# Kernel tuning notes

Measured on AMD Instinct MI355X. Metric: run time of the kernel, lower is better.

## Reference

```python
import jax, jax.numpy as jnp
import numpy as np
import math

B, S, D = 8, 4096, 64

def setup_inputs() -> dict:
    key = jax.random.key(0)
    k1, k2, k3 = jax.random.split(key, 3)
    value = jax.random.normal(k1, (B, S, D), dtype=jnp.float32)
    key_t = jax.random.normal(k2, (B, S, D), dtype=jnp.float32)
    query = jax.random.normal(k3, (B, S, D), dtype=jnp.float32)
    return {"value": value, "key": key_t, "query": query}

def reference(value, key, query):
    # scores[b, q, k] = sum_d query[b,q,d] * key[b,k,d]
    scores = jnp.einsum('bqd,bkd->bqk', query, key) / math.sqrt(query.shape[-1])
    # NOTE: softmax over dim=1 (the QUERY axis), matching the original torch code
    attn = jax.nn.softmax(scores, axis=1)
    # outputs[b, q, d] = sum_k attn[b,q,k] * value[b,k,d]
    return jnp.einsum('bqk,bkd->bqd', attn, value)
```

## Files before the change

kernel.cpp:

```cpp
#include <hip/hip_runtime.h>

#define Bn 8
#define Sn 4096
#define Dn 64

constexpr int NKT = Sn / 64;
constexpr int NQT = Sn / 128;

typedef _Float16 half_t;
typedef __attribute__((ext_vector_type(2))) _Float16 half2v;
typedef __attribute__((ext_vector_type(4))) _Float16 half4;
typedef __attribute__((ext_vector_type(8))) _Float16 half8;
typedef __attribute__((ext_vector_type(4))) float f32x4;

constexpr float SCALE = 0.125f;
constexpr float SCALE2 = 0.125f * 1.4426950408889634f;

#define MFMA32(a, b, c) __builtin_amdgcn_mfma_f32_16x16x32_f16((a), (b), (c), 0, 0, 0)
#define MFMA16(a, b, c) __builtin_amdgcn_mfma_f32_16x16x16f16((a), (b), (c), 0, 0, 0)

__device__ __forceinline__ float fexp2(float x) {
#if defined(__has_builtin) && __has_builtin(__builtin_amdgcn_exp2f)
  return __builtin_amdgcn_exp2f(x);
#else
  return exp2f(x);
#endif
}

__device__ __forceinline__ int swz_k(int row, int col) {
  return row * 64 + (col ^ ((row & 7) << 3));
}
__device__ __forceinline__ int swz_v(int row, int col) {
  return row * 64 + (col ^ (((row & 7) << 3) ^ (((row >> 3) & 7) << 2)));
}

__device__ __forceinline__ void cvt8(const float* s, half8& h, half8& l) {
  #pragma unroll
  for (int j = 0; j < 8; ++j) {
    half_t hh = (half_t)s[j];
    h[j] = hh;
    l[j] = (half_t)(s[j] - (float)hh);
  }
}

__device__ __forceinline__ void cp16(half_t* lds, const half_t* g) {
  __builtin_amdgcn_global_load_lds(
      (const __attribute__((address_space(1))) unsigned int*)g,
      (__attribute__((address_space(3))) unsigned int*)lds, 16, 0, 0);
}


__global__ __launch_bounds__(256, 2)
void prep_q(const float* __restrict__ Qg, half_t* __restrict__ QhW,
            half_t* __restrict__ QlW) {
  const int t = threadIdx.x;
  const int b = blockIdx.x & 7, qt = blockIdx.x >> 3;
  const float* Qb = Qg + ((size_t)(b * Sn + qt * 128)) * Dn;
  half_t* qh = QhW + ((size_t)(b * NQT + qt)) * 8192;
  half_t* ql = QlW + ((size_t)(b * NQT + qt)) * 8192;
  #pragma unroll
  for (int i = 0; i < 8; ++i) {
    int f = t + 256 * i, q = f >> 4, d4 = (f & 15) << 2;
    float4 v = *(const float4*)(Qb + (size_t)q * Dn + d4);
    float s4[4] = {v.x * SCALE2, v.y * SCALE2, v.z * SCALE2, v.w * SCALE2};
    half4 h, l;
    #pragma unroll
    for (int j = 0; j < 4; ++j) {
      half_t hh = (half_t)s4[j];
      h[j] = hh;
      l[j] = (half_t)(s4[j] - (float)hh);
    }
    *(half4*)&qh[swz_k(q, d4)] = h;
    *(half4*)&ql[swz_k(q, d4)] = l;
  }
}

__global__ __launch_bounds__(256, 2)
void attn_linv(const float* __restrict__ Kg, const float* __restrict__ Vg,
               const half_t* __restrict__ QhW, const half_t* __restrict__ QlW,
               float* __restrict__ lg2inv, half_t* __restrict__ KVW) {
  __shared__ alignas(16) half_t Qh_s[2][8192];
  __shared__ alignas(16) half_t Ql_s[2][8192];
  __shared__ alignas(16) float red[4][4][16];

  const int t = threadIdx.x;
  const int lane = t & 63, w = t >> 6, g = lane >> 4, c16 = lane & 15;
  const int b = blockIdx.x & 7, kx = blockIdx.x >> 3;
  const int k0 = kx * 64;

  half_t* blob = KVW + ((size_t)(b * NKT + kx)) * 12288;

  half8 kfh[4][2], kfl[4][2];
  #pragma unroll
  for (int ks = 0; ks < 4; ++ks)
    #pragma unroll
    for (int c = 0; c < 2; ++c) {
      const float* src = Kg + ((size_t)(b * Sn + k0 + 16 * ks + c16)) * Dn + 32 * c + 8 * g;
      float a8[8];
      *(float4*)&a8[0] = *(const float4*)src;
      *(float4*)&a8[4] = *(const float4*)(src + 4);
      cvt8(a8, kfh[ks][c], kfl[ks][c]);
    }
  {
    #pragma unroll
    for (int ks = 0; ks < 4; ++ks)
      if (ks == w) {
        #pragma unroll
        for (int c = 0; c < 2; ++c) {
          *(half8*)&blob[swz_k(16 * ks + c16, 32 * c + 8 * g)] = kfh[ks][c];
          *(half8*)&blob[4096 + swz_k(16 * ks + c16, 32 * c + 8 * g)] = kfl[ks][c];
        }
      }
  }
  {
    const float* Vb = Vg + ((size_t)(b * Sn + k0)) * Dn;
    #pragma unroll
    for (int i = 0; i < 2; ++i) {
      int u = t + 256 * i;
      int k2 = u >> 4, dg = u & 15;
      float4 v0 = *(const float4*)(Vb + (size_t)(2 * k2) * Dn + 4 * dg);
      float4 v1 = *(const float4*)(Vb + (size_t)(2 * k2 + 1) * Dn + 4 * dg);
      const float* v0p = (const float*)&v0;
      const float* v1p = (const float*)&v1;
      #pragma unroll
      for (int j = 0; j < 4; ++j) {
        half2v pair = {(half_t)v0p[j], (half_t)v1p[j]};
        *(half2v*)&blob[8192 + swz_v(4 * dg + j, 2 * k2)] = pair;
      }
    }
  }

  const half_t* qhw = QhW + (size_t)b * NQT * 8192;
  const half_t* qlw = QlW + (size_t)b * NQT * 8192;

  auto load_q = [&](int bb, int qt) {
    const size_t toff = (size_t)qt * 8192;
    #pragma unroll
    for (int c = 0; c < 4; ++c) {
      const int ch = (c * 4 + w) * 512;
      cp16(&Qh_s[bb][ch], qhw + toff + ch + lane * 8);
      cp16(&Ql_s[bb][ch], qlw + toff + ch + lane * 8);
    }
  };

  float lsum[4] = {0.f, 0.f, 0.f, 0.f};

  load_q(0, 0);
  __syncthreads();
  for (int qt = 0; qt < NQT; ++qt) {
    if (qt + 1 < NQT) load_q((qt + 1) & 1, qt + 1);
    const int cur = qt & 1;
    #pragma unroll
    for (int qs = 0; qs < 2; ++qs) {
      const int qloc = 32 * w + 16 * qs + c16;
      half8 qh[2], ql[2];
      #pragma unroll
      for (int c = 0; c < 2; ++c) {
        qh[c] = *(const half8*)&Qh_s[cur][swz_k(qloc, 32 * c + 8 * g)];
        ql[c] = *(const half8*)&Ql_s[cur][swz_k(qloc, 32 * c + 8 * g)];
      }
      #pragma unroll
      for (int ks = 0; ks < 4; ++ks) {
        f32x4 acc = {0.f, 0.f, 0.f, 0.f};
        acc = MFMA32(qh[0], kfh[ks][0], acc);
        acc = MFMA32(qh[1], kfh[ks][1], acc);
        acc = MFMA32(ql[0], kfh[ks][0], acc);
        acc = MFMA32(ql[1], kfh[ks][1], acc);
        acc = MFMA32(qh[0], kfl[ks][0], acc);
        acc = MFMA32(qh[1], kfl[ks][1], acc);
        lsum[ks] += fexp2(acc[0]) + fexp2(acc[1]) + fexp2(acc[2]) + fexp2(acc[3]);
      }
    }
    __syncthreads();
  }

  #pragma unroll
  for (int ks = 0; ks < 4; ++ks) {
    lsum[ks] += __shfl_xor(lsum[ks], 16);
    lsum[ks] += __shfl_xor(lsum[ks], 32);
  }
  __syncthreads();
  if (lane < 16) {
    #pragma unroll
    for (int ks = 0; ks < 4; ++ks) red[w][ks][lane] = lsum[ks];
  }
  __syncthreads();
  if (t < 64) {
    int ks = t >> 4, c = t & 15;
    float tot = red[0][ks][c] + red[1][ks][c] + red[2][ks][c] + red[3][ks][c];
    lg2inv[(size_t)b * Sn + k0 + 16 * ks + c] = -log2f(tot);
  }
}

__global__ __launch_bounds__(512, 4)
void attn_pv(const half_t* __restrict__ KVW, const float* __restrict__ Qg,
             const float* __restrict__ lg2inv, float* __restrict__ Og) {
  __shared__ alignas(16) half_t KV_s[2][12288];

  const int t = threadIdx.x;
  const int lane = t & 63, w = t >> 6;
  const int g = (lane >> 4) & 3, c16 = lane & 15;
  const int wk = w & 3, wq = w >> 2;
  const int b = blockIdx.x & 7;
  const int q0 = (blockIdx.x >> 3) * 64;

  half8 qh[2][2], ql[2][2];
  #pragma unroll
  for (int qs = 0; qs < 2; ++qs) {
    const int qrow = q0 + 32 * wq + 16 * qs + c16;
    #pragma unroll
    for (int c = 0; c < 2; ++c) {
      const float* src = Qg + ((size_t)(b * Sn + qrow)) * Dn + 32 * c + 8 * g;
      float a8[8];
      *(float4*)&a8[0] = *(const float4*)src;
      *(float4*)&a8[4] = *(const float4*)(src + 4);
      #pragma unroll
      for (int j = 0; j < 8; ++j) a8[j] *= SCALE2;
      cvt8(a8, qh[qs][c], ql[qs][c]);
    }
  }

  f32x4 accO[2][4];
  #pragma unroll
  for (int qs = 0; qs < 2; ++qs)
    #pragma unroll
    for (int ds = 0; ds < 4; ++ds) accO[qs][ds] = {0.f, 0.f, 0.f, 0.f};

  auto load_kv = [&](int bb, int kt) {
    const half_t* src = KVW + ((size_t)(b * NKT + kt)) * 12288;
    half_t* dst = KV_s[bb];
    cp16(dst + w * 512, src + w * 512 + lane * 8);
    cp16(dst + (8 + w) * 512, src + (8 + w) * 512 + lane * 8);
    cp16(dst + (16 + w) * 512, src + (16 + w) * 512 + lane * 8);
  };

  const int krow = 16 * wk + c16;
  const int okh0 = swz_k(krow, 8 * g);
  const int okh1 = swz_k(krow, 32 + 8 * g);
  const float* lgp = lg2inv + (size_t)b * Sn + 16 * wk + 4 * g;

  load_kv(0, 0);
  __syncthreads();
  for (int kt = 0; kt < NKT; ++kt) {
    if (kt + 1 < NKT) load_kv((kt + 1) & 1, kt + 1);
    const int cur = kt & 1;
    const half_t* KH = &KV_s[cur][0];
    const half_t* KL = &KV_s[cur][4096];
    const half_t* VT = &KV_s[cur][8192];

    half8 kh0 = *(const half8*)&KH[okh0];
    half8 kh1 = *(const half8*)&KH[okh1];
    half8 kl0 = *(const half8*)&KL[okh0];
    half8 kl1 = *(const half8*)&KL[okh1];
    f32x4 lg4 = *(const f32x4*)(lgp + (size_t)kt * 64);

    f32x4 sv[2];
    __builtin_amdgcn_s_setprio(1);
    #pragma unroll
    for (int qs = 0; qs < 2; ++qs) {
      f32x4 acc = {0.f, 0.f, 0.f, 0.f};
      acc = MFMA32(kh0, qh[qs][0], acc);
      acc = MFMA32(kh1, qh[qs][1], acc);
      acc = MFMA32(kh0, ql[qs][0], acc);
      acc = MFMA32(kh1, ql[qs][1], acc);
      acc = MFMA32(kl0, qh[qs][0], acc);
      acc = MFMA32(kl1, qh[qs][1], acc);
      sv[qs] = acc;
    }
    __builtin_amdgcn_s_setprio(0);

    half4 ph[2];
    #pragma unroll
    for (int qs = 0; qs < 2; ++qs) {
      float p0 = fexp2(sv[qs][0] + lg4[0]);
      float p1 = fexp2(sv[qs][1] + lg4[1]);
      float p2 = fexp2(sv[qs][2] + lg4[2]);
      float p3 = fexp2(sv[qs][3] + lg4[3]);
      ph[qs] = {(half_t)p0, (half_t)p1, (half_t)p2, (half_t)p3};
    }

    __builtin_amdgcn_s_setprio(1);
    #pragma unroll
    for (int ds = 0; ds < 4; ++ds) {
      half4 vt = *(const half4*)&VT[swz_v(16 * ds + c16, 16 * wk + 4 * g)];
      accO[0][ds] = MFMA16(vt, ph[0], accO[0][ds]);
      accO[1][ds] = MFMA16(vt, ph[1], accO[1][ds]);
    }
    __builtin_amdgcn_s_setprio(0);

    __syncthreads();
  }

  float* red = (float*)&KV_s[0][0];
  #pragma unroll
  for (int qs = 0; qs < 2; ++qs) {
    if (wk != 0) {
      #pragma unroll
      for (int ds = 0; ds < 4; ++ds)
        *(f32x4*)&red[(((wq * 3 + (wk - 1)) * 4) + ds) * 256 + lane * 4] = accO[qs][ds];
    }
    __syncthreads();
    if (wk == 0) {
      const int qrow = q0 + 32 * wq + 16 * qs + c16;
      float* Ob = Og + ((size_t)(b * Sn + qrow)) * Dn;
      #pragma unroll
      for (int ds = 0; ds < 4; ++ds) {
        f32x4 o = accO[qs][ds];
        #pragma unroll
        for (int j = 0; j < 3; ++j)
          o += *(const f32x4*)&red[(((wq * 3 + j) * 4) + ds) * 256 + lane * 4];
        *(f32x4*)(Ob + 16 * ds + 4 * g) = o;
      }
    }
    __syncthreads();
  }
}

__global__ __launch_bounds__(256, 2)
void fb_attn_linv(const float* __restrict__ Kg, const float* __restrict__ Qg,
                  float* __restrict__ linv) {
  __shared__ alignas(16) half_t Qh_s[128 * 64];
  __shared__ alignas(16) half_t Ql_s[128 * 64];
  __shared__ alignas(16) float red[4][4][16];

  const int t = threadIdx.x;
  const int lane = t & 63, w = t >> 6, g = lane >> 4, c16 = lane & 15;
  const int b = blockIdx.y;
  const int k0 = blockIdx.x * 64;

  half8 kfh[4][2], kfl[4][2];
  #pragma unroll
  for (int ks = 0; ks < 4; ++ks)
    #pragma unroll
    for (int c = 0; c < 2; ++c) {
      const float* src = Kg + ((size_t)(b * Sn + k0 + 16 * ks + c16)) * Dn + 32 * c + 8 * g;
      float a8[8];
      *(float4*)&a8[0] = *(const float4*)src;
      *(float4*)&a8[4] = *(const float4*)(src + 4);
      cvt8(a8, kfh[ks][c], kfl[ks][c]);
    }

  float lsum[4] = {0.f, 0.f, 0.f, 0.f};

  for (int q0 = 0; q0 < Sn; q0 += 128) {
    __syncthreads();
    const float* Qb = Qg + ((size_t)(b * Sn + q0)) * Dn;
    #pragma unroll
    for (int i = 0; i < 8; ++i) {
      int f = t + 256 * i, q = f >> 4, d4 = (f & 15) << 2;
      float4 v = *(const float4*)(Qb + (size_t)q * Dn + d4);
      float s4[4] = {v.x * SCALE, v.y * SCALE, v.z * SCALE, v.w * SCALE};
      half4 h, l;
      #pragma unroll
      for (int j = 0; j < 4; ++j) {
        half_t hh = (half_t)s4[j];
        h[j] = hh;
        l[j] = (half_t)(s4[j] - (float)hh);
      }
      *(half4*)&Qh_s[swz_k(q, d4)] = h;
      *(half4*)&Ql_s[swz_k(q, d4)] = l;
    }
    __syncthreads();

    #pragma unroll
    for (int qs = 0; qs < 2; ++qs) {
      const int qloc = 32 * w + 16 * qs + c16;
      half8 qh[2], ql[2];
      #pragma unroll
      for (int c = 0; c < 2; ++c) {
        qh[c] = *(const half8*)&Qh_s[swz_k(qloc, 32 * c + 8 * g)];
        ql[c] = *(const half8*)&Ql_s[swz_k(qloc, 32 * c + 8 * g)];
      }
      #pragma unroll
      for (int ks = 0; ks < 4; ++ks) {
        f32x4 acc = {0.f, 0.f, 0.f, 0.f};
        acc = MFMA32(qh[0], kfh[ks][0], acc);
        acc = MFMA32(qh[1], kfh[ks][1], acc);
        acc = MFMA32(ql[0], kfh[ks][0], acc);
        acc = MFMA32(ql[1], kfh[ks][1], acc);
        acc = MFMA32(qh[0], kfl[ks][0], acc);
        acc = MFMA32(qh[1], kfl[ks][1], acc);
        lsum[ks] += __expf(acc[0]) + __expf(acc[1]) + __expf(acc[2]) + __expf(acc[3]);
      }
    }
  }

  #pragma unroll
  for (int ks = 0; ks < 4; ++ks) {
    lsum[ks] += __shfl_xor(lsum[ks], 16);
    lsum[ks] += __shfl_xor(lsum[ks], 32);
  }
  __syncthreads();
  if (lane < 16) {
    #pragma unroll
    for (int ks = 0; ks < 4; ++ks) red[w][ks][lane] = lsum[ks];
  }
  __syncthreads();
  if (t < 64) {
    int ks = t >> 4, c = t & 15;
    float tot = red[0][ks][c] + red[1][ks][c] + red[2][ks][c] + red[3][ks][c];
    linv[(size_t)b * Sn + k0 + 16 * ks + c] = 1.0f / tot;
  }
}

__global__ __launch_bounds__(512, 2)
void fb_attn_pv(const float* __restrict__ Vg, const float* __restrict__ Kg,
                const float* __restrict__ Qg, const float* __restrict__ linv,
                float* __restrict__ Og) {
  __shared__ alignas(16) half_t Kh_s[64 * 64];
  __shared__ alignas(16) half_t Kl_s[64 * 64];
  __shared__ alignas(16) half_t Vt_s[64 * 64];
  __shared__ alignas(16) float li_s[64];
  __shared__ alignas(16) float red[4][2][4][256];

  const int t = threadIdx.x;
  const int lane = t & 63, w = t >> 6;
  const int g = (lane >> 4) & 3, c16 = lane & 15;
  const int wq = w & 3, wk = w >> 2;
  const int b = blockIdx.y;
  const int q0 = blockIdx.x * 128;

  half8 qh[2][2], ql[2][2];
  #pragma unroll
  for (int qs = 0; qs < 2; ++qs) {
    const int qrow = q0 + 32 * wq + 16 * qs + c16;
    #pragma unroll
    for (int c = 0; c < 2; ++c) {
      const float* src = Qg + ((size_t)(b * Sn + qrow)) * Dn + 32 * c + 8 * g;
      float a8[8];
      *(float4*)&a8[0] = *(const float4*)src;
      *(float4*)&a8[4] = *(const float4*)(src + 4);
      #pragma unroll
      for (int j = 0; j < 8; ++j) a8[j] *= SCALE;
      cvt8(a8, qh[qs][c], ql[qs][c]);
    }
  }

  f32x4 accO[2][4];
  #pragma unroll
  for (int qs = 0; qs < 2; ++qs)
    #pragma unroll
    for (int ds = 0; ds < 4; ++ds) accO[qs][ds] = {0.f, 0.f, 0.f, 0.f};

  const int krow0 = t >> 4, kd40 = (t & 15) << 2;
  const int krow1 = 32 + (t >> 4), kd41 = kd40;
  const int vk2 = t >> 4, vdg = t & 15;

  float4 kreg0, kreg1, vreg0, vreg1;
  float li_reg = 0.f;
  {
    const float* Kb = Kg + ((size_t)(b * Sn)) * Dn;
    const float* Vb = Vg + ((size_t)(b * Sn)) * Dn;
    kreg0 = *(const float4*)(Kb + (size_t)krow0 * Dn + kd40);
    kreg1 = *(const float4*)(Kb + (size_t)krow1 * Dn + kd41);
    vreg0 = *(const float4*)(Vb + (size_t)(2 * vk2) * Dn + 4 * vdg);
    vreg1 = *(const float4*)(Vb + (size_t)(2 * vk2 + 1) * Dn + 4 * vdg);
    if (t < 64) li_reg = linv[(size_t)b * Sn + t];
  }

  for (int kt = 0; kt < Sn / 64; ++kt) {
    __syncthreads();
    {
      const float* k0p = (const float*)&kreg0;
      const float* k1p = (const float*)&kreg1;
      half4 h, l;
      #pragma unroll
      for (int j = 0; j < 4; ++j) {
        half_t hh = (half_t)k0p[j];
        h[j] = hh; l[j] = (half_t)(k0p[j] - (float)hh);
      }
      *(half4*)&Kh_s[swz_k(krow0, kd40)] = h;
      *(half4*)&Kl_s[swz_k(krow0, kd40)] = l;
      #pragma unroll
      for (int j = 0; j < 4; ++j) {
        half_t hh = (half_t)k1p[j];
        h[j] = hh; l[j] = (half_t)(k1p[j] - (float)hh);
      }
      *(half4*)&Kh_s[swz_k(krow1, kd41)] = h;
      *(half4*)&Kl_s[swz_k(krow1, kd41)] = l;

      const float* v0p = (const float*)&vreg0;
      const float* v1p = (const float*)&vreg1;
      #pragma unroll
      for (int j = 0; j < 4; ++j) {
        half2v pair = {(half_t)v0p[j], (half_t)v1p[j]};
        *(half2v*)&Vt_s[swz_v(4 * vdg + j, 2 * vk2)] = pair;
      }
      if (t < 64) li_s[t] = li_reg;
    }
    __syncthreads();

    if (kt + 1 < Sn / 64) {
      const float* Kb = Kg + ((size_t)(b * Sn + (kt + 1) * 64)) * Dn;
      const float* Vb = Vg + ((size_t)(b * Sn + (kt + 1) * 64)) * Dn;
      kreg0 = *(const float4*)(Kb + (size_t)krow0 * Dn + kd40);
      kreg1 = *(const float4*)(Kb + (size_t)krow1 * Dn + kd41);
      vreg0 = *(const float4*)(Vb + (size_t)(2 * vk2) * Dn + 4 * vdg);
      vreg1 = *(const float4*)(Vb + (size_t)(2 * vk2 + 1) * Dn + 4 * vdg);
      if (t < 64) li_reg = linv[(size_t)b * Sn + (kt + 1) * 64 + t];
    }

    #pragma unroll
    for (int kss = 0; kss < 2; ++kss) {
      const int ks = 2 * wk + kss;
      const int krow = 16 * ks + c16;
      half8 kh0 = *(const half8*)&Kh_s[swz_k(krow, 8 * g)];
      half8 kh1 = *(const half8*)&Kh_s[swz_k(krow, 32 + 8 * g)];
      half8 kl0 = *(const half8*)&Kl_s[swz_k(krow, 8 * g)];
      half8 kl1 = *(const half8*)&Kl_s[swz_k(krow, 32 + 8 * g)];
      f32x4 li4 = *(const f32x4*)&li_s[16 * ks + 4 * g];

      half4 ph[2];
      #pragma unroll
      for (int qs = 0; qs < 2; ++qs) {
        f32x4 acc = {0.f, 0.f, 0.f, 0.f};
        acc = MFMA32(kh0, qh[qs][0], acc);
        acc = MFMA32(kh1, qh[qs][1], acc);
        acc = MFMA32(kh0, ql[qs][0], acc);
        acc = MFMA32(kh1, ql[qs][1], acc);
        acc = MFMA32(kl0, qh[qs][0], acc);
        acc = MFMA32(kl1, qh[qs][1], acc);
        float p0 = __expf(acc[0]) * li4[0];
        float p1 = __expf(acc[1]) * li4[1];
        float p2 = __expf(acc[2]) * li4[2];
        float p3 = __expf(acc[3]) * li4[3];
        ph[qs] = {(half_t)p0, (half_t)p1, (half_t)p2, (half_t)p3};
      }
      #pragma unroll
      for (int ds = 0; ds < 4; ++ds) {
        half4 vt = *(const half4*)&Vt_s[swz_v(16 * ds + c16, 16 * ks + 4 * g)];
        accO[0][ds] = MFMA16(vt, ph[0], accO[0][ds]);
        accO[1][ds] = MFMA16(vt, ph[1], accO[1][ds]);
      }
    }
  }

  if (wk == 1) {
    #pragma unroll
    for (int qs = 0; qs < 2; ++qs)
      #pragma unroll
      for (int ds = 0; ds < 4; ++ds)
        *(f32x4*)&red[wq][qs][ds][lane * 4] = accO[qs][ds];
  }
  __syncthreads();
  if (wk == 0) {
    #pragma unroll
    for (int qs = 0; qs < 2; ++qs) {
      const int qrow = q0 + 32 * wq + 16 * qs + c16;
      float* Ob = Og + ((size_t)(b * Sn + qrow)) * Dn;
      #pragma unroll
      for (int ds = 0; ds < 4; ++ds) {
        f32x4 o = accO[qs][ds] + *(const f32x4*)&red[wq][qs][ds][lane * 4];
        *(f32x4*)(Ob + 16 * ds + 4 * g) = o;
      }
    }
  }
}

extern "C" void kernel_launch(void* const* d_in, const int* in_sizes, int n_in,
                              void* d_out, int out_size, void* d_ws, size_t ws_size,
                              hipStream_t stream) {
  const float* V = reinterpret_cast<const float*>(d_in[0]);
  const float* K = reinterpret_cast<const float*>(d_in[1]);
  const float* Q = reinterpret_cast<const float*>(d_in[2]);
  float* O = reinterpret_cast<float*>(d_out);

  char* ws = reinterpret_cast<char*>(d_ws);
  const size_t MB = 1024 * 1024;
  const size_t WS_NEEDED = 21 * MB;

  float* li = reinterpret_cast<float*>(ws);
  if (ws_size >= WS_NEEDED) {
    half_t* QhW = reinterpret_cast<half_t*>(ws + 1 * MB);
    half_t* QlW = reinterpret_cast<half_t*>(ws + 5 * MB);
    half_t* KVW = reinterpret_cast<half_t*>(ws + 9 * MB);
    prep_q<<<dim3(NQT * Bn), dim3(256), 0, stream>>>(Q, QhW, QlW);
    attn_linv<<<dim3(NKT * Bn), dim3(256), 0, stream>>>(K, V, QhW, QlW, li, KVW);
    attn_pv<<<dim3((Sn / 64) * Bn), dim3(512), 0, stream>>>(KVW, Q, li, O);
  } else {
    fb_attn_linv<<<dim3(Sn / 64, Bn), dim3(256), 0, stream>>>(K, Q, li);
    fb_attn_pv<<<dim3(Sn / 128, Bn), dim3(512), 0, stream>>>(V, K, Q, li, O);
  }
}
```

Measured before the change: 133.4 us.

## Give each wave a private KV slice and drop per-tile block barriers

Reorganizes the packed K/V tile layout so each 16-key group forms a contiguous per-wave slice. In the PV kernel, each wave now streams its own slice into a double-buffered LDS region and waits only on its own async copies via s_waitcnt vmcnt, removing the __syncthreads at every key tile. The cost is doubled LDS per block, duplicate global loads for the two waves that share a key group, one wasted wrap-around prefetch, and a launch bound lowered from 4 to 2 blocks, which reduces occupancy.

```diff
diff --git a/kernel.cpp b/kernel.cpp
--- a/kernel.cpp
+++ b/kernel.cpp
@@ -107,8 +107,9 @@
       if (ks == w) {
         #pragma unroll
         for (int c = 0; c < 2; ++c) {
-          *(half8*)&blob[swz_k(16 * ks + c16, 32 * c + 8 * g)] = kfh[ks][c];
-          *(half8*)&blob[4096 + swz_k(16 * ks + c16, 32 * c + 8 * g)] = kfl[ks][c];
+          const int off = c16 * 64 + ((32 * c + 8 * g) ^ ((c16 & 7) << 3));
+          *(half8*)&blob[ks * 3072 + off] = kfh[ks][c];
+          *(half8*)&blob[ks * 3072 + 1024 + off] = kfl[ks][c];
         }
       }
   }
@@ -122,10 +123,12 @@
       float4 v1 = *(const float4*)(Vb + (size_t)(2 * k2 + 1) * Dn + 4 * dg);
       const float* v0p = (const float*)&v0;
       const float* v1p = (const float*)&v1;
+      const int wk = k2 >> 3;
+      const int kloc = (2 * k2) & 15;
       #pragma unroll
       for (int j = 0; j < 4; ++j) {
         half2v pair = {(half_t)v0p[j], (half_t)v1p[j]};
-        *(half2v*)&blob[8192 + swz_v(4 * dg + j, 2 * k2)] = pair;
+        *(half2v*)&blob[wk * 3072 + 2048 + (4 * dg + j) * 16 + kloc] = pair;
       }
     }
   }
@@ -192,10 +195,10 @@
   }
 }
 
-__global__ __launch_bounds__(512, 4)
+__global__ __launch_bounds__(512, 2)
 void attn_pv(const half_t* __restrict__ KVW, const float* __restrict__ Qg,
              const float* __restrict__ lg2inv, float* __restrict__ Og) {
-  __shared__ alignas(16) half_t KV_s[2][12288];
+  __shared__ alignas(16) half_t KV_s[2][24576];
 
   const int t = threadIdx.x;
   const int lane = t & 63, w = t >> 6;
@@ -203,6 +206,7 @@
   const int wk = w & 3, wq = w >> 2;
   const int b = blockIdx.x & 7;
   const int q0 = (blockIdx.x >> 3) * 64;
+  const int wslice = w * 3072;
 
   half8 qh[2][2], ql[2][2];
   #pragma unroll
@@ -227,32 +231,23 @@
     for (int ds = 0; ds < 4; ++ds) accO[qs][ds] = {0.f, 0.f, 0.f, 0.f};
 
   auto load_kv = [&](int bb, int kt) {
-    const half_t* src = KVW + ((size_t)(b * NKT + kt)) * 12288;
-    half_t* dst = KV_s[bb];
-    cp16(dst + w * 512, src + w * 512 + lane * 8);
-    cp16(dst + (8 + w) * 512, src + (8 + w) * 512 + lane * 8);
-    cp16(dst + (16 + w) * 512, src + (16 + w) * 512 + lane * 8);
+    const half_t* src = KVW + ((size_t)(b * NKT + kt)) * 12288 + wk * 3072;
+    half_t* dst = &KV_s[bb][wslice];
+    #pragma unroll
+    for (int i = 0; i < 6; ++i)
+      cp16(dst + i * 512, src + i * 512 + lane * 8);
   };
 
-  const int krow = 16 * wk + c16;
-  const int okh0 = swz_k(krow, 8 * g);
-  const int okh1 = swz_k(krow, 32 + 8 * g);
+  const int okh0 = c16 * 64 + ((8 * g) ^ ((c16 & 7) << 3));
+  const int okh1 = c16 * 64 + ((32 + 8 * g) ^ ((c16 & 7) << 3));
   const float* lgp = lg2inv + (size_t)b * Sn + 16 * wk + 4 * g;
 
-  load_kv(0, 0);
-  __syncthreads();
-  for (int kt = 0; kt < NKT; ++kt) {
-    if (kt + 1 < NKT) load_kv((kt + 1) & 1, kt + 1);
-    const int cur = kt & 1;
-    const half_t* KH = &KV_s[cur][0];
-    const half_t* KL = &KV_s[cur][4096];
-    const half_t* VT = &KV_s[cur][8192];
-
-    half8 kh0 = *(const half8*)&KH[okh0];
-    half8 kh1 = *(const half8*)&KH[okh1];
-    half8 kl0 = *(const half8*)&KL[okh0];
-    half8 kl1 = *(const half8*)&KL[okh1];
-    f32x4 lg4 = *(const f32x4*)(lgp + (size_t)kt * 64);
+  auto compute = [&](int bb, f32x4 lg) {
+    const half_t* S = &KV_s[bb][wslice];
+    half8 kh0 = *(const half8*)&S[okh0];
+    half8 kh1 = *(const half8*)&S[okh1];
+    half8 kl0 = *(const half8*)&S[1024 + okh0];
+    half8 kl1 = *(const half8*)&S[1024 + okh1];
 
     f32x4 sv[2];
     __builtin_amdgcn_s_setprio(1);
@@ -272,24 +267,46 @@
     half4 ph[2];
     #pragma unroll
     for (int qs = 0; qs < 2; ++qs) {
-      float p0 = fexp2(sv[qs][0] + lg4[0]);
-      float p1 = fexp2(sv[qs][1] + lg4[1]);
-      float p2 = fexp2(sv[qs][2] + lg4[2]);
-      float p3 = fexp2(sv[qs][3] + lg4[3]);
+      float p0 = fexp2(sv[qs][0] + lg[0]);
+      float p1 = fexp2(sv[qs][1] + lg[1]);
+      float p2 = fexp2(sv[qs][2] + lg[2]);
+      float p3 = fexp2(sv[qs][3] + lg[3]);
       ph[qs] = {(half_t)p0, (half_t)p1, (half_t)p2, (half_t)p3};
     }
 
     __builtin_amdgcn_s_setprio(1);
     #pragma unroll
     for (int ds = 0; ds < 4; ++ds) {
-      half4 vt = *(const half4*)&VT[swz_v(16 * ds + c16, 16 * wk + 4 * g)];
+      half4 vt = *(const half4*)&S[2048 + (16 * ds + c16) * 16 + 4 * g];
       accO[0][ds] = MFMA16(vt, ph[0], accO[0][ds]);
       accO[1][ds] = MFMA16(vt, ph[1], accO[1][ds]);
     }
     __builtin_amdgcn_s_setprio(0);
-
-    __syncthreads();
-  }
+  };
+
+  load_kv(0, 0);
+  f32x4 lgA = *(const f32x4*)lgp;
+  f32x4 lgB;
+
+  for (int kt = 0; kt < NKT; kt += 2) {
+    {
+      const int nk = (kt + 1 < NKT) ? kt + 1 : 0;
+      load_kv(1, nk);
+      lgB = *(const f32x4*)(lgp + (size_t)nk * 64);
+      asm volatile("s_waitcnt vmcnt(7)" ::: "memory");
+      compute(0, lgA);
+    }
+    {
+      const int nk = (kt + 2 < NKT) ? kt + 2 : 0;
+      load_kv(0, nk);
+      lgA = *(const f32x4*)(lgp + (size_t)nk * 64);
+      asm volatile("s_waitcnt vmcnt(7)" ::: "memory");
+      compute(1, lgB);
+    }
+  }
+
+  asm volatile("s_waitcnt vmcnt(0)" ::: "memory");
+  __syncthreads();
 
   float* red = (float*)&KV_s[0][0];
   #pragma unroll
```

After: 143.3 us. 7.5% more time.
